# Performance work log

Measured on AMD Instinct MI355X. Metric: run time of the kernel, lower is better.

Reference implementation:

```python
import jax, jax.numpy as jnp
import numpy as np
from jax import lax

B, S, H, L, O = 32, 512, 1024, 3, 1024


def _gru_layer(x, h0, Wzx, bz, Wzh, Wrx, br, Wrh, Wgx, bg, Wgh):
    # x: [B,S,H]; precompute all input-side gate projections as big GEMMs
    Xz = jnp.einsum('bsi,hi->bsh', x, Wzx) + bz  # [B,S,H]
    Xr = jnp.einsum('bsi,hi->bsh', x, Wrx) + br
    Xg = jnp.einsum('bsi,hi->bsh', x, Wgx) + bg

    def step(h, inp):
        xz, xr, xg = inp  # each [B,H]
        z = jax.nn.sigmoid(xz + h @ Wzh.T)
        r = jax.nn.sigmoid(xr + h @ Wrh.T)
        g = jnp.tanh(xg + (r * h) @ Wgh.T)
        h_new = z * h + (1.0 - z) * g
        return h_new, h_new

    xs = (Xz.transpose(1, 0, 2), Xr.transpose(1, 0, 2), Xg.transpose(1, 0, 2))  # [S,B,H]
    hT, ys = lax.scan(step, h0, xs)
    return ys.transpose(1, 0, 2), hT  # [B,S,H], [B,H]


def setup_inputs() -> dict:
    key = jax.random.key(0)
    ks = jax.random.split(key, 12)
    sc = 0.02
    inp = {
        'x': jax.random.normal(ks[0], (B, S, H), jnp.float32),
        'h0': jnp.zeros((B, L, H), jnp.float32),
        # stacked per-layer GRU weights (layer input dim == H for all layers)
        'Wzx': jax.random.normal(ks[1], (L, H, H), jnp.float32) * sc,
        'bz': jax.random.normal(ks[2], (L, H), jnp.float32) * sc,
        'Wzh': jax.random.normal(ks[3], (L, H, H), jnp.float32) * sc,
        'Wrx': jax.random.normal(ks[4], (L, H, H), jnp.float32) * sc,
        'br': jax.random.normal(ks[5], (L, H), jnp.float32) * sc,
        'Wrh': jax.random.normal(ks[6], (L, H, H), jnp.float32) * sc,
        'Wgx': jax.random.normal(ks[7], (L, H, H), jnp.float32) * sc,
        'bg': jax.random.normal(ks[8], (L, H), jnp.float32) * sc,
        'Wgh': jax.random.normal(ks[9], (L, H, H), jnp.float32) * sc,
        'Wo': jax.random.normal(ks[10], (O, H), jnp.float32) * sc,
        'bo': jax.random.normal(ks[11], (O,), jnp.float32) * sc,
    }
    return inp


def reference(x, h0, Wzx, bz, Wzh, Wrx, br, Wrh, Wgx, bg, Wgh, Wo, bo):
    layer_in = x
    finals = []
    for l in range(L):  # small fixed layer count
        layer_in, hT = _gru_layer(layer_in, h0[:, l, :], Wzx[l], bz[l], Wzh[l],
                                  Wrx[l], br[l], Wrh[l], Wgx[l], bg[l], Wgh[l])
        finals.append(hT)
    hidden_state = jnp.stack(finals, axis=1)  # [B,L,H]
    layer_output = jnp.einsum('bsh,oh->bso', layer_in, Wo) + bo  # [B,S,O]
    return layer_output, hidden_state
```

## Files before the change

kernel.cpp:

```cpp
#include <hip/hip_runtime.h>
#include <hip/hip_bf16.h>
#include <math.h>


#define BB 32
#define SS 512
#define HH 1024
#define LL 3
#define OO 1024
#define SH (SS*HH)

typedef __attribute__((ext_vector_type(8))) short short8;
typedef __attribute__((ext_vector_type(4))) float float4v;
typedef unsigned long long u64;
typedef unsigned int u32;
typedef unsigned short u16;

__device__ __forceinline__ u16 f2bf(float f) {
  union { float f; u32 u; } v; v.f = f;
  return (u16)((v.u + 0x7FFFu + ((v.u >> 16) & 1u)) >> 16);
}

__global__ void convert_bf16(const float* __restrict__ src,
                             u16* __restrict__ dst, int n) {
  int stride = gridDim.x * blockDim.x;
  for (int i = blockIdx.x * blockDim.x + threadIdx.x; i < n; i += stride)
    dst[i] = f2bf(src[i]);
}

__global__ void pack_w(const float* __restrict__ src, u16* __restrict__ dst,
                       int nmat) {
  int stride = gridDim.x * blockDim.x;
  int total = nmat * 1048576;
  for (int i = blockIdx.x * blockDim.x + threadIdx.x; i < total; i += stride) {
    int m = i >> 20, e = i & 1048575;
    int row = e >> 10, k = e & 1023;
    int lane = ((k >> 3) & 3) * 16 + (row & 15);
    int di = ((row >> 4) * 32 + (k >> 5)) * 512 + lane * 8 + (k & 7);
    dst[m * 1048576 + di] = f2bf(src[i]);
  }
}

__global__ void pack_x(const float* __restrict__ x, u16* __restrict__ dst) {
  int stride = gridDim.x * blockDim.x;
  for (int d = blockIdx.x * blockDim.x + threadIdx.x; d < SS * 32768; d += stride) {
    int t = d >> 15, e = d & 32767;
    int rt = e >> 14, ks = (e >> 9) & 31, lane = (e >> 3) & 63, j = e & 7;
    int b = rt * 16 + (lane & 15), c = ks * 32 + ((lane >> 4) << 3) + j;
    dst[d] = f2bf(x[(size_t)b * SH + (size_t)t * HH + c]);
  }
}

__global__ void pack_h0(const float* __restrict__ h0, u16* __restrict__ y0,
                        u16* __restrict__ y1, u16* __restrict__ y2) {
  int i = blockIdx.x * 256 + threadIdx.x;
  int l = i >> 15, e = i & 32767;
  int rt = e >> 14, ks = (e >> 9) & 31, lane = (e >> 3) & 63, j = e & 7;
  int b = rt * 16 + (lane & 15), c = ks * 32 + ((lane >> 4) << 3) + j;
  u16 v = f2bf(h0[b * (LL * HH) + l * HH + c]);
  u16* dst = (l == 0) ? y0 : ((l == 1) ? y1 : y2);
  dst[e] = v;
}

__device__ __forceinline__ short8 coh16(const u16* p) {
  const u64* q = (const u64*)p;
  union { u64 q[2]; short8 v; } u;
  u.q[0] = __hip_atomic_load(q,     __ATOMIC_RELAXED, __HIP_MEMORY_SCOPE_AGENT);
  u.q[1] = __hip_atomic_load(q + 1, __ATOMIC_RELAXED, __HIP_MEMORY_SCOPE_AGENT);
  return u.v;
}
__device__ __forceinline__ void coh_store16(u16* p, short8 v) {
  asm volatile("global_store_dwordx4 %0, %1, off sc0 sc1"
               :: "v"(p), "v"(v) : "memory");
}
__device__ __forceinline__ void coh_store_u32(int* p, int v) {
  asm volatile("global_store_dword %0, %1, off sc0 sc1"
               :: "v"(p), "v"(v) : "memory");
}
__device__ __forceinline__ void poll2(const int* base, int lane, int tgt) {
  const int* p0 = base + lane;
  const int* p1 = base + 64 + lane;
  int f0 = __hip_atomic_load(p0, __ATOMIC_RELAXED, __HIP_MEMORY_SCOPE_AGENT);
  int f1 = __hip_atomic_load(p1, __ATOMIC_RELAXED, __HIP_MEMORY_SCOPE_AGENT);
  while (__any((f0 < tgt) | (f1 < tgt))) {
    __builtin_amdgcn_s_sleep(1);
    f0 = __hip_atomic_load(p0, __ATOMIC_RELAXED, __HIP_MEMORY_SCOPE_AGENT);
    f1 = __hip_atomic_load(p1, __ATOMIC_RELAXED, __HIP_MEMORY_SCOPE_AGENT);
  }
}

#define MFMA16(a, b, c) __builtin_amdgcn_mfma_f32_16x16x32_bf16(a, b, c, 0, 0, 0)

__launch_bounds__(256, 1)
__global__ void gru_pipe(
    const u16* __restrict__ xpk0,
    u16* __restrict__ ypk0, u16* __restrict__ ypk1, u16* __restrict__ ypk2,
    const u16* __restrict__ Pzh, const u16* __restrict__ Pzx,
    const u16* __restrict__ Prh, const u16* __restrict__ Prx,
    const u16* __restrict__ Pgh, const u16* __restrict__ Pgx,
    const float* __restrict__ bz, const float* __restrict__ br,
    const float* __restrict__ bg, const float* __restrict__ h0,
    u16* __restrict__ rhA, float* __restrict__ hid,
    int* __restrict__ flagsD, int* __restrict__ flagsP) {
  __shared__ __align__(16) u16 smW[3][16384];
  __shared__ float redz[4][2][64], redr[4][2][64], redg[4][2][64];
  __shared__ __align__(16) u16 pubP[2][256];

  const int grp = blockIdx.x >> 6;
  const int blk = blockIdx.x & 63;
  const int tid = threadIdx.x;
  const int lane = tid & 63;
  const int wave = tid >> 6;
  const int mt = wave & 1;
  const int kh = wave >> 1;
  const int fcol = lane & 15, kg = lane >> 4;
  const int crow0 = mt * 16 + kg * 4;
  const int colZ = blk * 16 + fcol;

  u16* ypkl       = (grp == 0) ? ypk0 : ((grp == 1) ? ypk1 : ypk2);
  const u16* ypkp = (grp == 1) ? ypk0 : ypk1;
  const bool circ = (grp < 2);
  const size_t lw = (size_t)grp * 1048576;
  const u16* wZx = Pzx + lw + blk * 16384 + lane * 8;
  const u16* wRx = Prx + lw + blk * 16384 + lane * 8;
  const u16* wGx = Pgx + lw + blk * 16384 + lane * 8;
  u16* rhl = rhA + grp * (BB * HH);
  int* selfD = flagsD + (grp + 1) * 128;
  int* prodD = flagsD + grp * 128;
  int* consD = flagsD + (grp + 2) * 128;
  int* selfP = flagsP + grp * 128;

  {
    const u64* g0 = (const u64*)(Pzh + lw + blk * 16384);
    const u64* g1 = (const u64*)(Prh + lw + blk * 16384);
    const u64* g2 = (const u64*)(Pgh + lw + blk * 16384);
    u64* d0 = (u64*)smW[0];
    u64* d1 = (u64*)smW[1];
    u64* d2 = (u64*)smW[2];
#pragma unroll
    for (int j = 0; j < 16; ++j) {
      d0[j * 256 + tid] = g0[j * 256 + tid];
      d1[j * 256 + tid] = g1[j * 256 + tid];
      d2[j * 256 + tid] = g2[j * 256 + tid];
    }
  }
  __syncthreads();
  const u16* lZ = smW[0] + lane * 8;
  const u16* lR = smW[1] + lane * 8;
  const u16* lG = smW[2] + lane * 8;

  float hreg[4] = {0, 0, 0, 0}, zreg[4] = {0, 0, 0, 0};
  float bzv = 0, brv = 0, bgv = 0;
  if (kh == 0) {
#pragma unroll
    for (int q = 0; q < 4; ++q)
      hreg[q] = h0[(crow0 + q) * (LL * HH) + grp * HH + colZ];
    bzv = bz[grp * HH + colZ];
    brv = br[grp * HH + colZ];
    bgv = bg[grp * HH + colZ];
  }

  const int pubOff = (mt * 32 + (blk >> 1)) * 512 + (blk & 1) * 256;

  for (int t = 0; t < SS; ++t) {
    const int hslot = circ ? (t & 127) : t;
    const int wslot = circ ? ((t + 1) & 127) : (t + 1);

    if (kh == 0) {
      poll2(selfD, lane, t);
      if (circ && t >= 128) poll2(consD, lane, t - 127);
    } else if (grp != 0) {
      poll2(prodD, lane, t + 1);
    }

    float4v az0 = {0,0,0,0}, az1 = {0,0,0,0};
    float4v ar0 = {0,0,0,0}, ar1 = {0,0,0,0};
    float4v ag0 = {0,0,0,0}, ag1 = {0,0,0,0};
    short8 cf[16];

    if (kh == 0) {
      const u16* hbase = ypkl + (size_t)hslot * 32768 + mt * 16384 + lane * 8;
#pragma unroll
      for (int c0 = 0; c0 < 32; c0 += 16) {
#pragma unroll
        for (int k = 0; k < 16; ++k)
          cf[k] = coh16(hbase + (c0 + k) * 512);
#pragma unroll
        for (int k = 0; k < 16; ++k) {
          short8 vz = *(const short8*)(lZ + (c0 + k) * 512);
          short8 vr = *(const short8*)(lR + (c0 + k) * 512);
          if (k & 1) { az1 = MFMA16(cf[k], vz, az1); ar1 = MFMA16(cf[k], vr, ar1); }
          else       { az0 = MFMA16(cf[k], vz, az0); ar0 = MFMA16(cf[k], vr, ar0); }
        }
      }
    } else {
      const u16* xbase = (grp == 0)
          ? (xpk0 + (size_t)t * 32768 + mt * 16384 + lane * 8)
          : (ypkp + (size_t)((t + 1) & 127) * 32768 + mt * 16384 + lane * 8);
#pragma unroll
      for (int c0 = 0; c0 < 32; c0 += 16) {
        if (grp != 0) {
#pragma unroll
          for (int k = 0; k < 16; ++k) cf[k] = coh16(xbase + (c0 + k) * 512);
        } else {
#pragma unroll
          for (int k = 0; k < 16; ++k) cf[k] = *(const short8*)(xbase + (c0 + k) * 512);
        }
#pragma unroll
        for (int k = 0; k < 16; ++k) {
          int ks = c0 + k;
          short8 vz = *(const short8*)(wZx + ks * 512);
          short8 vr = *(const short8*)(wRx + ks * 512);
          short8 vg = *(const short8*)(wGx + ks * 512);
          if (k & 1) { az1 = MFMA16(cf[k], vz, az1); ar1 = MFMA16(cf[k], vr, ar1);
                       ag1 = MFMA16(cf[k], vg, ag1); }
          else       { az0 = MFMA16(cf[k], vz, az0); ar0 = MFMA16(cf[k], vr, ar0);
                       ag0 = MFMA16(cf[k], vg, ag0); }
        }
      }
#pragma unroll
      for (int q = 0; q < 4; ++q) {
        redz[q][mt][lane] = az0[q] + az1[q];
        redr[q][mt][lane] = ar0[q] + ar1[q];
      }
    }
    __syncthreads();

    if (kh == 0) {
#pragma unroll
      for (int q = 0; q < 4; ++q) {
        float pz = az0[q] + az1[q] + redz[q][mt][lane] + bzv;
        float pr = ar0[q] + ar1[q] + redr[q][mt][lane] + brv;
        zreg[q] = 1.f / (1.f + expf(-pz));
        float rv = 1.f / (1.f + expf(-pr));
        pubP[mt][(((fcol >> 3) << 4) + kg * 4 + q) * 8 + (fcol & 7)] =
            f2bf(rv * hreg[q]);
      }
      asm volatile("s_waitcnt lgkmcnt(0)" ::: "memory");
      __builtin_amdgcn_sched_barrier(0);
      if (lane < 32) {
        short8 v = *(const short8*)(pubP[mt] + lane * 8);
        coh_store16(rhl + pubOff + lane * 8, v);
      }
      asm volatile("s_waitcnt vmcnt(0)" ::: "memory");
      if (lane == 0) coh_store_u32(selfP + blk * 2 + mt, t + 1);
    }

    poll2(selfP, lane, t + 1);

    {
      const u16* rbase = rhl + mt * 16384 + kh * 8192 + lane * 8;
#pragma unroll
      for (int k = 0; k < 16; ++k) cf[k] = coh16(rbase + k * 512);
#pragma unroll
      for (int k = 0; k < 16; ++k) {
        short8 vg = *(const short8*)(lG + (kh * 16 + k) * 512);
        if (k & 1) ag1 = MFMA16(cf[k], vg, ag1);
        else       ag0 = MFMA16(cf[k], vg, ag0);
      }
    }
    if (kh == 1) {
#pragma unroll
      for (int q = 0; q < 4; ++q) redg[q][mt][lane] = ag0[q] + ag1[q];
    }
    __syncthreads();

    if (kh == 0) {
#pragma unroll
      for (int q = 0; q < 4; ++q) {
        float pg = ag0[q] + ag1[q] + redg[q][mt][lane] + bgv;
        float gv = tanhf(pg);
        float hn = zreg[q] * hreg[q] + (1.f - zreg[q]) * gv;
        hreg[q] = hn;
        pubP[mt][(((fcol >> 3) << 4) + kg * 4 + q) * 8 + (fcol & 7)] = f2bf(hn);
        if (t == SS - 1) hid[(crow0 + q) * (LL * HH) + grp * HH + colZ] = hn;
      }
      asm volatile("s_waitcnt lgkmcnt(0)" ::: "memory");
      __builtin_amdgcn_sched_barrier(0);
      if (lane < 32) {
        short8 v = *(const short8*)(pubP[mt] + lane * 8);
        coh_store16(ypkl + (size_t)wslot * 32768 + pubOff + lane * 8, v);
      }
      asm volatile("s_waitcnt vmcnt(0)" ::: "memory");
      if (lane == 0) coh_store_u32(selfD + blk * 2 + mt, t + 1);
    }
  }
}

__launch_bounds__(64)
__global__ void out_gemm(const u16* __restrict__ ypk2, const u16* __restrict__ W,
                         const float* __restrict__ bo, float* __restrict__ C) {
  const int lane = threadIdx.x;
  const int nt4 = blockIdx.x & 15;
  const int sb = blockIdx.x >> 4;
  const int s = sb >> 1, bt = sb & 1;
  const int n0 = nt4 * 64;
  const int fcol = lane & 15, kg = lane >> 4;
  const u16* Abase = ypk2 + (size_t)(s + 1) * 32768 + bt * 16384 + lane * 8;
  float4v acc[4];
#pragma unroll
  for (int j = 0; j < 4; ++j) acc[j] = (float4v){0, 0, 0, 0};

  for (int ks = 0; ks < 32; ++ks) {
    short8 a = *(const short8*)(Abase + ks * 512);
#pragma unroll
    for (int j = 0; j < 4; ++j) {
      short8 b = *(const short8*)(W + (size_t)(n0 + j * 16 + fcol) * HH + ks * 32 + kg * 8);
      acc[j] = MFMA16(a, b, acc[j]);
    }
  }
#pragma unroll
  for (int j = 0; j < 4; ++j)
#pragma unroll
    for (int q = 0; q < 4; ++q) {
      int b = bt * 16 + kg * 4 + q;
      int col = n0 + j * 16 + fcol;
      C[((size_t)b * SS + s) * OO + col] = acc[j][q] + bo[col];
    }
}

extern "C" void kernel_launch(void* const* d_in, const int* in_sizes, int n_in,
                              void* d_out, int out_size, void* d_ws, size_t ws_size,
                              hipStream_t stream) {
  (void)in_sizes; (void)n_in; (void)out_size; (void)ws_size;

  const float* x   = (const float*)d_in[0];
  const float* h0  = (const float*)d_in[1];
  const float* Wzx = (const float*)d_in[2];
  const float* bz  = (const float*)d_in[3];
  const float* Wzh = (const float*)d_in[4];
  const float* Wrx = (const float*)d_in[5];
  const float* br  = (const float*)d_in[6];
  const float* Wrh = (const float*)d_in[7];
  const float* Wgx = (const float*)d_in[8];
  const float* bg  = (const float*)d_in[9];
  const float* Wgh = (const float*)d_in[10];
  const float* Wo  = (const float*)d_in[11];
  const float* bo  = (const float*)d_in[12];
  float* out = (float*)d_out;

  u16* Pzh = (u16*)d_ws;
  u16* Pzx = Pzh + 3145728;
  u16* Prh = Pzx + 3145728;
  u16* Prx = Prh + 3145728;
  u16* Pgh = Prx + 3145728;
  u16* Pgx = Pgh + 3145728;
  u16* Wob = Pgx + 3145728;
  u16* xpk0 = Wob + 1048576;
  u16* ypk0 = xpk0 + 16777216;
  u16* ypk1 = ypk0 + 128 * 32768;
  u16* ypk2 = ypk1 + 128 * 32768;
  u16* rhA  = ypk2 + 513 * 32768;
  int* flagsD = (int*)(rhA + 3 * 32768);
  int* flagsP = flagsD + 640;

  hipMemsetAsync(flagsD, 0x7F, 128 * sizeof(int), stream);
  hipMemsetAsync(flagsD + 128, 0, 512 * sizeof(int), stream);
  hipMemsetAsync(flagsP, 0, 384 * sizeof(int), stream);

  pack_w<<<3072, 256, 0, stream>>>(Wzh, Pzh, 3);
  pack_w<<<3072, 256, 0, stream>>>(Wzx, Pzx, 3);
  pack_w<<<3072, 256, 0, stream>>>(Wrh, Prh, 3);
  pack_w<<<3072, 256, 0, stream>>>(Wrx, Prx, 3);
  pack_w<<<3072, 256, 0, stream>>>(Wgh, Pgh, 3);
  pack_w<<<3072, 256, 0, stream>>>(Wgx, Pgx, 3);
  convert_bf16<<<256, 256, 0, stream>>>(Wo, Wob, 1048576);
  pack_x<<<4096, 256, 0, stream>>>(x, xpk0);
  pack_h0<<<384, 256, 0, stream>>>(h0, ypk0, ypk1, ypk2);

  gru_pipe<<<192, 256, 0, stream>>>(
      xpk0, ypk0, ypk1, ypk2,
      Pzh, Pzx, Prh, Prx, Pgh, Pgx,
      bz, br, bg, h0, rhA, out + 16777216, flagsD, flagsP);

  out_gemm<<<16384, 64, 0, stream>>>(ypk2, Wob, bo, out);
}
```

Before: 10.44 ms.

## Halve GRU pipeline blocks, give each block 32 columns, drop LDS weight cache

The persistent GRU pipeline kernel now runs 32 blocks per layer instead of 64. Each block computes two 16-column tiles, and flag polling shrinks from 128 to 64 flags per stage. The intent is to cut cross-block synchronisation and polling cost on the latency-bound recurrence. In exchange, each block does twice the MFMA work per step. The recurrent weights are no longer cached in shared memory and are streamed from global/L2 every timestep, which raises memory traffic on the critical path.

```diff
diff --git a/kernel.cpp b/kernel.cpp
--- a/kernel.cpp
+++ b/kernel.cpp
@@ -9,6 +9,7 @@
 #define LL 3
 #define OO 1024
 #define SH (SS*HH)
+#define NBL 32
 
 typedef __attribute__((ext_vector_type(8))) short short8;
 typedef __attribute__((ext_vector_type(4))) float float4v;
@@ -77,15 +78,13 @@
   asm volatile("global_store_dword %0, %1, off sc0 sc1"
                :: "v"(p), "v"(v) : "memory");
 }
-__device__ __forceinline__ void poll2(const int* base, int lane, int tgt) {
-  const int* p0 = base + lane;
-  const int* p1 = base + 64 + lane;
-  int f0 = __hip_atomic_load(p0, __ATOMIC_RELAXED, __HIP_MEMORY_SCOPE_AGENT);
-  int f1 = __hip_atomic_load(p1, __ATOMIC_RELAXED, __HIP_MEMORY_SCOPE_AGENT);
-  while (__any((f0 < tgt) | (f1 < tgt))) {
+__device__ __forceinline__ void poll64(const int* base, int lane, int tgt) {
+  int f = __hip_atomic_load(base + lane, __ATOMIC_RELAXED,
+                            __HIP_MEMORY_SCOPE_AGENT);
+  while (__any(f < tgt)) {
     __builtin_amdgcn_s_sleep(1);
-    f0 = __hip_atomic_load(p0, __ATOMIC_RELAXED, __HIP_MEMORY_SCOPE_AGENT);
-    f1 = __hip_atomic_load(p1, __ATOMIC_RELAXED, __HIP_MEMORY_SCOPE_AGENT);
+    f = __hip_atomic_load(base + lane, __ATOMIC_RELAXED,
+                          __HIP_MEMORY_SCOPE_AGENT);
   }
 }
 
@@ -102,12 +101,11 @@
     const float* __restrict__ bg, const float* __restrict__ h0,
     u16* __restrict__ rhA, float* __restrict__ hid,
     int* __restrict__ flagsD, int* __restrict__ flagsP) {
-  __shared__ __align__(16) u16 smW[3][16384];
-  __shared__ float redz[4][2][64], redr[4][2][64], redg[4][2][64];
-  __shared__ __align__(16) u16 pubP[2][256];
-
-  const int grp = blockIdx.x >> 6;
-  const int blk = blockIdx.x & 63;
+  __shared__ float redz[2][4][2][64], redr[2][4][2][64], redg[2][4][2][64];
+  __shared__ __align__(16) u16 pubP[2][512];
+
+  const int grp = blockIdx.x >> 5;
+  const int blk = blockIdx.x & 31;
   const int tid = threadIdx.x;
   const int lane = tid & 63;
   const int wave = tid >> 6;
@@ -115,138 +113,123 @@
   const int kh = wave >> 1;
   const int fcol = lane & 15, kg = lane >> 4;
   const int crow0 = mt * 16 + kg * 4;
-  const int colZ = blk * 16 + fcol;
+  const int colA = blk * 32 + fcol;
 
   u16* ypkl       = (grp == 0) ? ypk0 : ((grp == 1) ? ypk1 : ypk2);
   const u16* ypkp = (grp == 1) ? ypk0 : ypk1;
   const bool circ = (grp < 2);
   const size_t lw = (size_t)grp * 1048576;
-  const u16* wZx = Pzx + lw + blk * 16384 + lane * 8;
-  const u16* wRx = Prx + lw + blk * 16384 + lane * 8;
-  const u16* wGx = Pgx + lw + blk * 16384 + lane * 8;
-  u16* rhl = rhA + grp * (BB * HH);
-  int* selfD = flagsD + (grp + 1) * 128;
-  int* prodD = flagsD + grp * 128;
-  int* consD = flagsD + (grp + 2) * 128;
-  int* selfP = flagsP + grp * 128;
-
-  {
-    const u64* g0 = (const u64*)(Pzh + lw + blk * 16384);
-    const u64* g1 = (const u64*)(Prh + lw + blk * 16384);
-    const u64* g2 = (const u64*)(Pgh + lw + blk * 16384);
-    u64* d0 = (u64*)smW[0];
-    u64* d1 = (u64*)smW[1];
-    u64* d2 = (u64*)smW[2];
-#pragma unroll
-    for (int j = 0; j < 16; ++j) {
-      d0[j * 256 + tid] = g0[j * 256 + tid];
-      d1[j * 256 + tid] = g1[j * 256 + tid];
-      d2[j * 256 + tid] = g2[j * 256 + tid];
-    }
-  }
-  __syncthreads();
-  const u16* lZ = smW[0] + lane * 8;
-  const u16* lR = smW[1] + lane * 8;
-  const u16* lG = smW[2] + lane * 8;
-
-  float hreg[4] = {0, 0, 0, 0}, zreg[4] = {0, 0, 0, 0};
-  float bzv = 0, brv = 0, bgv = 0;
+  const u16 *w1z[2], *w1r[2], *wgx[2], *wgh[2];
+#pragma unroll
+  for (int s = 0; s < 2; ++s) {
+    const int nb = blk * 2 + s;
+    w1z[s] = (kh ? Pzx : Pzh) + lw + nb * 16384 + lane * 8;
+    w1r[s] = (kh ? Prx : Prh) + lw + nb * 16384 + lane * 8;
+    wgx[s] = Pgx + lw + nb * 16384 + lane * 8;
+    wgh[s] = Pgh + lw + nb * 16384 + lane * 8;
+  }
+  u16* rhl = rhA + grp * 32768;
+  int* selfD = flagsD + (grp + 1) * 64;
+  int* prodD = flagsD + grp * 64;
+  int* consD = flagsD + (grp + 2) * 64;
+  int* selfP = flagsP + grp * 64;
+
+  float hreg[2][4], zreg[2][4];
+  float bzv[2] = {0, 0}, brv[2] = {0, 0}, bgv[2] = {0, 0};
   if (kh == 0) {
 #pragma unroll
-    for (int q = 0; q < 4; ++q)
-      hreg[q] = h0[(crow0 + q) * (LL * HH) + grp * HH + colZ];
-    bzv = bz[grp * HH + colZ];
-    brv = br[grp * HH + colZ];
-    bgv = bg[grp * HH + colZ];
-  }
-
-  const int pubOff = (mt * 32 + (blk >> 1)) * 512 + (blk & 1) * 256;
+    for (int s = 0; s < 2; ++s) {
+#pragma unroll
+      for (int q = 0; q < 4; ++q)
+        hreg[s][q] = h0[(crow0 + q) * (LL * HH) + grp * HH + colA + s * 16];
+      bzv[s] = bz[grp * HH + colA + s * 16];
+      brv[s] = br[grp * HH + colA + s * 16];
+      bgv[s] = bg[grp * HH + colA + s * 16];
+    }
+  }
 
   for (int t = 0; t < SS; ++t) {
     const int hslot = circ ? (t & 127) : t;
     const int wslot = circ ? ((t + 1) & 127) : (t + 1);
 
     if (kh == 0) {
-      poll2(selfD, lane, t);
-      if (circ && t >= 128) poll2(consD, lane, t - 127);
+      poll64(selfD, lane, t);
+      if (circ && t >= 128) poll64(consD, lane, t - 127);
     } else if (grp != 0) {
-      poll2(prodD, lane, t + 1);
-    }
-
-    float4v az0 = {0,0,0,0}, az1 = {0,0,0,0};
-    float4v ar0 = {0,0,0,0}, ar1 = {0,0,0,0};
-    float4v ag0 = {0,0,0,0}, ag1 = {0,0,0,0};
+      poll64(prodD, lane, t + 1);
+    }
+
+    float4v az[2], ar[2], ag[2];
+#pragma unroll
+    for (int s = 0; s < 2; ++s) {
+      az[s] = (float4v){0,0,0,0}; ar[s] = (float4v){0,0,0,0};
+      ag[s] = (float4v){0,0,0,0};
+    }
     short8 cf[16];
 
+    const u16* Ab = (kh == 0)
+        ? (ypkl + (size_t)hslot * 32768 + mt * 16384 + lane * 8)
+        : ((grp != 0)
+            ? (ypkp + (size_t)((t + 1) & 127) * 32768 + mt * 16384 + lane * 8)
+            : (xpk0 + (size_t)t * 32768 + mt * 16384 + lane * 8));
+    const bool Acoh = (kh == 0) || (grp != 0);
+
+#pragma unroll
+    for (int c0 = 0; c0 < 32; c0 += 16) {
+      if (Acoh) {
+#pragma unroll
+        for (int k = 0; k < 16; ++k) cf[k] = coh16(Ab + (c0 + k) * 512);
+      } else {
+#pragma unroll
+        for (int k = 0; k < 16; ++k) cf[k] = *(const short8*)(Ab + (c0 + k) * 512);
+      }
+#pragma unroll
+      for (int k = 0; k < 16; ++k) {
+        const int ks = c0 + k;
+        az[0] = MFMA16(cf[k], *(const short8*)(w1z[0] + ks * 512), az[0]);
+        az[1] = MFMA16(cf[k], *(const short8*)(w1z[1] + ks * 512), az[1]);
+        ar[0] = MFMA16(cf[k], *(const short8*)(w1r[0] + ks * 512), ar[0]);
+        ar[1] = MFMA16(cf[k], *(const short8*)(w1r[1] + ks * 512), ar[1]);
+        if (kh) {
+          ag[0] = MFMA16(cf[k], *(const short8*)(wgx[0] + ks * 512), ag[0]);
+          ag[1] = MFMA16(cf[k], *(const short8*)(wgx[1] + ks * 512), ag[1]);
+        }
+      }
+    }
+    if (kh) {
+#pragma unroll
+      for (int s = 0; s < 2; ++s)
+#pragma unroll
+        for (int q = 0; q < 4; ++q) {
+          redz[s][q][mt][lane] = az[s][q];
+          redr[s][q][mt][lane] = ar[s][q];
+        }
+    }
+    __syncthreads();
+
     if (kh == 0) {
-      const u16* hbase = ypkl + (size_t)hslot * 32768 + mt * 16384 + lane * 8;
-#pragma unroll
-      for (int c0 = 0; c0 < 32; c0 += 16) {
-#pragma unroll
-        for (int k = 0; k < 16; ++k)
-          cf[k] = coh16(hbase + (c0 + k) * 512);
-#pragma unroll
-        for (int k = 0; k < 16; ++k) {
-          short8 vz = *(const short8*)(lZ + (c0 + k) * 512);
-          short8 vr = *(const short8*)(lR + (c0 + k) * 512);
-          if (k & 1) { az1 = MFMA16(cf[k], vz, az1); ar1 = MFMA16(cf[k], vr, ar1); }
-          else       { az0 = MFMA16(cf[k], vz, az0); ar0 = MFMA16(cf[k], vr, ar0); }
+#pragma unroll
+      for (int s = 0; s < 2; ++s)
+#pragma unroll
+        for (int q = 0; q < 4; ++q) {
+          float pz = az[s][q] + redz[s][q][mt][lane] + bzv[s];
+          float pr = ar[s][q] + redr[s][q][mt][lane] + brv[s];
+          zreg[s][q] = 1.f / (1.f + expf(-pz));
+          float rv = 1.f / (1.f + expf(-pr));
+          pubP[mt][((s * 2 + (fcol >> 3)) * 16 + kg * 4 + q) * 8 + (fcol & 7)] =
+              f2bf(rv * hreg[s][q]);
         }
-      }
-    } else {
-      const u16* xbase = (grp == 0)
-          ? (xpk0 + (size_t)t * 32768 + mt * 16384 + lane * 8)
-          : (ypkp + (size_t)((t + 1) & 127) * 32768 + mt * 16384 + lane * 8);
-#pragma unroll
-      for (int c0 = 0; c0 < 32; c0 += 16) {
-        if (grp != 0) {
-#pragma unroll
-          for (int k = 0; k < 16; ++k) cf[k] = coh16(xbase + (c0 + k) * 512);
-        } else {
-#pragma unroll
-          for (int k = 0; k < 16; ++k) cf[k] = *(const short8*)(xbase + (c0 + k) * 512);
-        }
-#pragma unroll
-        for (int k = 0; k < 16; ++k) {
-          int ks = c0 + k;
-          short8 vz = *(const short8*)(wZx + ks * 512);
-          short8 vr = *(const short8*)(wRx + ks * 512);
-          short8 vg = *(const short8*)(wGx + ks * 512);
-          if (k & 1) { az1 = MFMA16(cf[k], vz, az1); ar1 = MFMA16(cf[k], vr, ar1);
-                       ag1 = MFMA16(cf[k], vg, ag1); }
-          else       { az0 = MFMA16(cf[k], vz, az0); ar0 = MFMA16(cf[k], vr, ar0);
-                       ag0 = MFMA16(cf[k], vg, ag0); }
-        }
-      }
-#pragma unroll
-      for (int q = 0; q < 4; ++q) {
-        redz[q][mt][lane] = az0[q] + az1[q];
-        redr[q][mt][lane] = ar0[q] + ar1[q];
-      }
-    }
-    __syncthreads();
-
-    if (kh == 0) {
-#pragma unroll
-      for (int q = 0; q < 4; ++q) {
-        float pz = az0[q] + az1[q] + redz[q][mt][lane] + bzv;
-        float pr = ar0[q] + ar1[q] + redr[q][mt][lane] + brv;
-        zreg[q] = 1.f / (1.f + expf(-pz));
-        float rv = 1.f / (1.f + expf(-pr));
-        pubP[mt][(((fcol >> 3) << 4) + kg * 4 + q) * 8 + (fcol & 7)] =
-            f2bf(rv * hreg[q]);
-      }
       asm volatile("s_waitcnt lgkmcnt(0)" ::: "memory");
       __builtin_amdgcn_sched_barrier(0);
-      if (lane < 32) {
+      {
         short8 v = *(const short8*)(pubP[mt] + lane * 8);
-        coh_store16(rhl + pubOff + lane * 8, v);
+        coh_store16(rhl + (mt * 32 + blk) * 512 + lane * 8, v);
       }
       asm volatile("s_waitcnt vmcnt(0)" ::: "memory");
       if (lane == 0) coh_store_u32(selfP + blk * 2 + mt, t + 1);
     }
 
-    poll2(selfP, lane, t + 1);
+    poll64(selfP, lane, t + 1);
 
     {
       const u16* rbase = rhl + mt * 16384 + kh * 8192 + lane * 8;
@@ -254,32 +237,38 @@
       for (int k = 0; k < 16; ++k) cf[k] = coh16(rbase + k * 512);
 #pragma unroll
       for (int k = 0; k < 16; ++k) {
-        short8 vg = *(const short8*)(lG + (kh * 16 + k) * 512);
-        if (k & 1) ag1 = MFMA16(cf[k], vg, ag1);
-        else       ag0 = MFMA16(cf[k], vg, ag0);
-      }
-    }
-    if (kh == 1) {
-#pragma unroll
-      for (int q = 0; q < 4; ++q) redg[q][mt][lane] = ag0[q] + ag1[q];
+        const int ks = kh * 16 + k;
+        ag[0] = MFMA16(cf[k], *(const short8*)(wgh[0] + ks * 512), ag[0]);
+        ag[1] = MFMA16(cf[k], *(const short8*)(wgh[1] + ks * 512), ag[1]);
+      }
+    }
+    if (kh) {
+#pragma unroll
+      for (int s = 0; s < 2; ++s)
+#pragma unroll
+        for (int q = 0; q < 4; ++q) redg[s][q][mt][lane] = ag[s][q];
     }
     __syncthreads();
 
     if (kh == 0) {
 #pragma unroll
-      for (int q = 0; q < 4; ++q) {
-        float pg = ag0[q] + ag1[q] + redg[q][mt][lane] + bgv;
-        float gv = tanhf(pg);
-        float hn = zreg[q] * hreg[q] + (1.f - zreg[q]) * gv;
-        hreg[q] = hn;
-        pubP[mt][(((fcol >> 3) << 4) + kg * 4 + q) * 8 + (fcol & 7)] = f2bf(hn);
-        if (t == SS - 1) hid[(crow0 + q) * (LL * HH) + grp * HH + colZ] = hn;
-      }
+      for (int s = 0; s < 2; ++s)
+#pragma unroll
+        for (int q = 0; q < 4; ++q) {
+          float pg = ag[s][q] + redg[s][q][mt][lane] + bgv[s];
+          float gv = tanhf(pg);
+          float hn = zreg[s][q] * hreg[s][q] + (1.f - zreg[s][q]) * gv;
+          hreg[s][q] = hn;
+          pubP[mt][((s * 2 + (fcol >> 3)) * 16 + kg * 4 + q) * 8 + (fcol & 7)] =
+              f2bf(hn);
+          if (t == SS - 1)
+            hid[(crow0 + q) * (LL * HH) + grp * HH + colA + s * 16] = hn;
+        }
       asm volatile("s_waitcnt lgkmcnt(0)" ::: "memory");
       __builtin_amdgcn_sched_barrier(0);
-      if (lane < 32) {
+      {
         short8 v = *(const short8*)(pubP[mt] + lane * 8);
-        coh_store16(ypkl + (size_t)wslot * 32768 + pubOff + lane * 8, v);
+        coh_store16(ypkl + (size_t)wslot * 32768 + (mt * 32 + blk) * 512 + lane * 8, v);
       }
       asm volatile("s_waitcnt vmcnt(0)" ::: "memory");
       if (lane == 0) coh_store_u32(selfD + blk * 2 + mt, t + 1);
@@ -352,11 +341,9 @@
   u16* ypk2 = ypk1 + 128 * 32768;
   u16* rhA  = ypk2 + 513 * 32768;
   int* flagsD = (int*)(rhA + 3 * 32768);
-  int* flagsP = flagsD + 640;
-
-  hipMemsetAsync(flagsD, 0x7F, 128 * sizeof(int), stream);
-  hipMemsetAsync(flagsD + 128, 0, 512 * sizeof(int), stream);
-  hipMemsetAsync(flagsP, 0, 384 * sizeof(int), stream);
+  int* flagsP = flagsD + 256;
+
+  hipMemsetAsync(flagsD, 0, (256 + 192) * sizeof(int), stream);
 
   pack_w<<<3072, 256, 0, stream>>>(Wzh, Pzh, 3);
   pack_w<<<3072, 256, 0, stream>>>(Wzx, Pzx, 3);
@@ -368,7 +355,7 @@
   pack_x<<<4096, 256, 0, stream>>>(x, xpk0);
   pack_h0<<<384, 256, 0, stream>>>(h0, ypk0, ypk1, ypk2);
 
-  gru_pipe<<<192, 256, 0, stream>>>(
+  gru_pipe<<<96, 256, 0, stream>>>(
       xpk0, ypk0, ypk1, ypk2,
       Pzh, Pzx, Prh, Prx, Pgh, Pgx,
       bz, br, bg, h0, rhA, out + 16777216, flagsD, flagsP);
```

After: 34.94 ms. +234.8%, slower.

## Speculatively load and compute before flag check, recompute if not ready

Applied to the files above, without the earlier changes.

Instead of spinning on inter-block flags before loading shared state, each wave takes one snapshot of the flags and then immediately loads data and runs the MFMAs. If the snapshot showed not-ready, it polls and redoes the load and compute. Flags are split per row-tile (mt), so each wave polls only 64 flags instead of 128. The aim is to hide flag-check latency on the critical recurrent path. The cost is possible duplicated compute and loads when data arrives late, plus more code and register pressure.

```diff
diff --git a/kernel.cpp b/kernel.cpp
--- a/kernel.cpp
+++ b/kernel.cpp
@@ -69,6 +69,9 @@
   u.q[1] = __hip_atomic_load(q + 1, __ATOMIC_RELAXED, __HIP_MEMORY_SCOPE_AGENT);
   return u.v;
 }
+__device__ __forceinline__ int aloadi(const int* p) {
+  return __hip_atomic_load(p, __ATOMIC_RELAXED, __HIP_MEMORY_SCOPE_AGENT);
+}
 __device__ __forceinline__ void coh_store16(u16* p, short8 v) {
   asm volatile("global_store_dwordx4 %0, %1, off sc0 sc1"
                :: "v"(p), "v"(v) : "memory");
@@ -77,15 +80,11 @@
   asm volatile("global_store_dword %0, %1, off sc0 sc1"
                :: "v"(p), "v"(v) : "memory");
 }
-__device__ __forceinline__ void poll2(const int* base, int lane, int tgt) {
-  const int* p0 = base + lane;
-  const int* p1 = base + 64 + lane;
-  int f0 = __hip_atomic_load(p0, __ATOMIC_RELAXED, __HIP_MEMORY_SCOPE_AGENT);
-  int f1 = __hip_atomic_load(p1, __ATOMIC_RELAXED, __HIP_MEMORY_SCOPE_AGENT);
-  while (__any((f0 < tgt) | (f1 < tgt))) {
+__device__ __forceinline__ void poll64(const int* base, int lane, int tgt) {
+  int f = aloadi(base + lane);
+  while (__any(f < tgt)) {
     __builtin_amdgcn_s_sleep(1);
-    f0 = __hip_atomic_load(p0, __ATOMIC_RELAXED, __HIP_MEMORY_SCOPE_AGENT);
-    f1 = __hip_atomic_load(p1, __ATOMIC_RELAXED, __HIP_MEMORY_SCOPE_AGENT);
+    f = aloadi(base + lane);
   }
 }
 
@@ -124,11 +123,11 @@
   const u16* wZx = Pzx + lw + blk * 16384 + lane * 8;
   const u16* wRx = Prx + lw + blk * 16384 + lane * 8;
   const u16* wGx = Pgx + lw + blk * 16384 + lane * 8;
-  u16* rhl = rhA + grp * (BB * HH);
-  int* selfD = flagsD + (grp + 1) * 128;
-  int* prodD = flagsD + grp * 128;
-  int* consD = flagsD + (grp + 2) * 128;
-  int* selfP = flagsP + grp * 128;
+  u16* rhl = rhA + grp * 32768;
+  int* selfD = flagsD + (grp + 1) * 128 + mt * 64;
+  int* prodD = flagsD + grp * 128 + mt * 64;
+  int* consD = flagsD + (grp + 2) * 128 + mt * 64;
+  int* selfP = flagsP + grp * 128 + mt * 64;
 
   {
     const u64* g0 = (const u64*)(Pzh + lw + blk * 16384);
@@ -166,57 +165,85 @@
     const int hslot = circ ? (t & 127) : t;
     const int wslot = circ ? ((t + 1) & 127) : (t + 1);
 
-    if (kh == 0) {
-      poll2(selfD, lane, t);
-      if (circ && t >= 128) poll2(consD, lane, t - 127);
-    } else if (grp != 0) {
-      poll2(prodD, lane, t + 1);
-    }
-
     float4v az0 = {0,0,0,0}, az1 = {0,0,0,0};
     float4v ar0 = {0,0,0,0}, ar1 = {0,0,0,0};
     float4v ag0 = {0,0,0,0}, ag1 = {0,0,0,0};
     short8 cf[16];
 
     if (kh == 0) {
+      bool ready;
+      {
+        int f0 = aloadi(selfD + lane);
+        bool r0 = !__any(f0 < t);
+        bool r1 = true;
+        if (circ && t >= 128) {
+          int f1 = aloadi(consD + lane);
+          r1 = !__any(f1 < t - 127);
+        }
+        ready = r0 && r1;
+      }
+      __builtin_amdgcn_sched_barrier(0);
       const u16* hbase = ypkl + (size_t)hslot * 32768 + mt * 16384 + lane * 8;
-#pragma unroll
-      for (int c0 = 0; c0 < 32; c0 += 16) {
-#pragma unroll
-        for (int k = 0; k < 16; ++k)
-          cf[k] = coh16(hbase + (c0 + k) * 512);
-#pragma unroll
-        for (int k = 0; k < 16; ++k) {
-          short8 vz = *(const short8*)(lZ + (c0 + k) * 512);
-          short8 vr = *(const short8*)(lR + (c0 + k) * 512);
-          if (k & 1) { az1 = MFMA16(cf[k], vz, az1); ar1 = MFMA16(cf[k], vr, ar1); }
-          else       { az0 = MFMA16(cf[k], vz, az0); ar0 = MFMA16(cf[k], vr, ar0); }
+      for (int a = 0; a < 2; ++a) {
+        az0 = (float4v){0,0,0,0}; az1 = (float4v){0,0,0,0};
+        ar0 = (float4v){0,0,0,0}; ar1 = (float4v){0,0,0,0};
+#pragma unroll
+        for (int c0 = 0; c0 < 32; c0 += 16) {
+#pragma unroll
+          for (int k = 0; k < 16; ++k) cf[k] = coh16(hbase + (c0 + k) * 512);
+#pragma unroll
+          for (int k = 0; k < 16; ++k) {
+            short8 vz = *(const short8*)(lZ + (c0 + k) * 512);
+            short8 vr = *(const short8*)(lR + (c0 + k) * 512);
+            if (k & 1) { az1 = MFMA16(cf[k], vz, az1); ar1 = MFMA16(cf[k], vr, ar1); }
+            else       { az0 = MFMA16(cf[k], vz, az0); ar0 = MFMA16(cf[k], vr, ar0); }
+          }
         }
+        if (ready) break;
+        poll64(selfD, lane, t);
+        if (circ && t >= 128) poll64(consD, lane, t - 127);
+        __builtin_amdgcn_sched_barrier(0);
+        ready = true;
       }
     } else {
+      bool ready = true;
+      if (grp != 0) {
+        int f0 = aloadi(prodD + lane);
+        ready = !__any(f0 < t + 1);
+      }
+      __builtin_amdgcn_sched_barrier(0);
       const u16* xbase = (grp == 0)
           ? (xpk0 + (size_t)t * 32768 + mt * 16384 + lane * 8)
           : (ypkp + (size_t)((t + 1) & 127) * 32768 + mt * 16384 + lane * 8);
-#pragma unroll
-      for (int c0 = 0; c0 < 32; c0 += 16) {
-        if (grp != 0) {
-#pragma unroll
-          for (int k = 0; k < 16; ++k) cf[k] = coh16(xbase + (c0 + k) * 512);
-        } else {
-#pragma unroll
-          for (int k = 0; k < 16; ++k) cf[k] = *(const short8*)(xbase + (c0 + k) * 512);
+      for (int a = 0; a < 2; ++a) {
+        az0 = (float4v){0,0,0,0}; az1 = (float4v){0,0,0,0};
+        ar0 = (float4v){0,0,0,0}; ar1 = (float4v){0,0,0,0};
+        ag0 = (float4v){0,0,0,0}; ag1 = (float4v){0,0,0,0};
+#pragma unroll
+        for (int c0 = 0; c0 < 32; c0 += 16) {
+          if (grp != 0) {
+#pragma unroll
+            for (int k = 0; k < 16; ++k) cf[k] = coh16(xbase + (c0 + k) * 512);
+          } else {
+#pragma unroll
+            for (int k = 0; k < 16; ++k) cf[k] = *(const short8*)(xbase + (c0 + k) * 512);
+          }
+#pragma unroll
+          for (int k = 0; k < 16; ++k) {
+            int ks = c0 + k;
+            short8 vz = *(const short8*)(wZx + ks * 512);
+            short8 vr = *(const short8*)(wRx + ks * 512);
+            short8 vg = *(const short8*)(wGx + ks * 512);
+            if (k & 1) { az1 = MFMA16(cf[k], vz, az1); ar1 = MFMA16(cf[k], vr, ar1);
+                         ag1 = MFMA16(cf[k], vg, ag1); }
+            else       { az0 = MFMA16(cf[k], vz, az0); ar0 = MFMA16(cf[k], vr, ar0);
+                         ag0 = MFMA16(cf[k], vg, ag0); }
+          }
         }
-#pragma unroll
-        for (int k = 0; k < 16; ++k) {
-          int ks = c0 + k;
-          short8 vz = *(const short8*)(wZx + ks * 512);
-          short8 vr = *(const short8*)(wRx + ks * 512);
-          short8 vg = *(const short8*)(wGx + ks * 512);
-          if (k & 1) { az1 = MFMA16(cf[k], vz, az1); ar1 = MFMA16(cf[k], vr, ar1);
-                       ag1 = MFMA16(cf[k], vg, ag1); }
-          else       { az0 = MFMA16(cf[k], vz, az0); ar0 = MFMA16(cf[k], vr, ar0);
-                       ag0 = MFMA16(cf[k], vg, ag0); }
-        }
+        if (ready) break;
+        poll64(prodD, lane, t + 1);
+        __builtin_amdgcn_sched_barrier(0);
+        ready = true;
       }
 #pragma unroll
       for (int q = 0; q < 4; ++q) {
@@ -243,20 +270,32 @@
         coh_store16(rhl + pubOff + lane * 8, v);
       }
       asm volatile("s_waitcnt vmcnt(0)" ::: "memory");
-      if (lane == 0) coh_store_u32(selfP + blk * 2 + mt, t + 1);
-    }
-
-    poll2(selfP, lane, t + 1);
+      if (lane == 0) coh_store_u32(selfP + blk, t + 1);
+    }
 
     {
+      bool ready;
+      {
+        int f0 = aloadi(selfP + lane);
+        ready = !__any(f0 < t + 1);
+      }
+      __builtin_amdgcn_sched_barrier(0);
+      const float4v ag0s = ag0, ag1s = ag1;
       const u16* rbase = rhl + mt * 16384 + kh * 8192 + lane * 8;
-#pragma unroll
-      for (int k = 0; k < 16; ++k) cf[k] = coh16(rbase + k * 512);
-#pragma unroll
-      for (int k = 0; k < 16; ++k) {
-        short8 vg = *(const short8*)(lG + (kh * 16 + k) * 512);
-        if (k & 1) ag1 = MFMA16(cf[k], vg, ag1);
-        else       ag0 = MFMA16(cf[k], vg, ag0);
+      for (int a = 0; a < 2; ++a) {
+        ag0 = ag0s; ag1 = ag1s;
+#pragma unroll
+        for (int k = 0; k < 16; ++k) cf[k] = coh16(rbase + k * 512);
+#pragma unroll
+        for (int k = 0; k < 16; ++k) {
+          short8 vg = *(const short8*)(lG + (kh * 16 + k) * 512);
+          if (k & 1) ag1 = MFMA16(cf[k], vg, ag1);
+          else       ag0 = MFMA16(cf[k], vg, ag0);
+        }
+        if (ready) break;
+        poll64(selfP, lane, t + 1);
+        __builtin_amdgcn_sched_barrier(0);
+        ready = true;
       }
     }
     if (kh == 1) {
@@ -282,7 +321,7 @@
         coh_store16(ypkl + (size_t)wslot * 32768 + pubOff + lane * 8, v);
       }
       asm volatile("s_waitcnt vmcnt(0)" ::: "memory");
-      if (lane == 0) coh_store_u32(selfD + blk * 2 + mt, t + 1);
+      if (lane == 0) coh_store_u32(selfD + blk, t + 1);
     }
   }
 }
```

Result: slower. 26.31 ms (+152.1%).
